# Optimization experiments

Measured on AMD Instinct MI355X. Metric: run time of the kernel, lower is better.

The kernel has to match this reference:

```python
import jax, jax.numpy as jnp
import numpy as np

T = 4096      # tokens (flattened batch*seq)
DIN = 2048    # input hidden dim
DQ = 2048     # q output dim
DKV = 2048    # per-head-group kv output dim (== DQ here, MHA)
NA = 4        # number of adapters (LoRA/delta models)
R = 16        # lora rank per q/k/v


def setup_inputs() -> dict:
    key = jax.random.key(0)
    ks = jax.random.split(key, 8)
    def rn(k, shape, scale):
        return jax.random.normal(k, shape, dtype=jnp.float32) * scale
    return {
        "x": rn(ks[0], (T, DIN), 1.0),
        "W_base": rn(ks[1], (DQ + 2 * DKV, DIN), DIN ** -0.5),
        "A_buffer_qkv": rn(ks[2], (NA, DIN, 3 * R), DIN ** -0.5),
        "B_buffer_q": rn(ks[3], (NA, R, DQ), R ** -0.5),
        "B_buffer_kv": rn(ks[4], (NA, R, 2 * DKV), R ** -0.5),
        "DeltaW_q": rn(ks[5], (NA, DIN, DQ), DIN ** -0.5),
        "DeltaW_kv": rn(ks[6], (NA, DIN, 2 * DKV), DIN ** -0.5),
        "weight_indices": jax.random.randint(ks[7], (T,), 0, NA, dtype=jnp.int32),
    }


def _ldmm(indices, x, A, B, D):
    """Per-token adapter-indexed (LoRA + dense delta) matmul.
    indices: [T] int, x: [T, din], A: [na, din, r], B: [na, r, dout], D: [na, din, dout].
    out[t] = (x[t] @ A[a]) @ B[a] + x[t] @ D[a]  with a = indices[t].
    Implemented as masked GEMMs over the small fixed adapter set.
    """
    na = A.shape[0]
    out = jnp.zeros((x.shape[0], B.shape[2]), dtype=x.dtype)
    for a in range(na):  # small fixed loop over adapters
        xa = jnp.where((indices == a)[:, None], x, jnp.zeros((), x.dtype))
        out = out + (xa @ A[a]) @ B[a] + xa @ D[a]
    return out


def reference(x, W_base, A_buffer_qkv, B_buffer_q, B_buffer_kv,
              DeltaW_q, DeltaW_kv, weight_indices):
    # base QKV projection (ColumnParallelLinear, no bias): [T, dq + 2*dkv]
    base = x @ W_base.T
    rank = A_buffer_qkv.shape[2] // 3
    b_dim_q = B_buffer_q.shape[2]
    b_dim_kv = B_buffer_kv.shape[2] // 2
    d_dim_kv = DeltaW_kv.shape[2] // 2
    for i in range(3):  # q, k, v slices
        if i == 0:
            o = _ldmm(weight_indices, x,
                      A_buffer_qkv[:, :, :rank], B_buffer_q, DeltaW_q)
            base = base.at[:, :b_dim_q].add(o)
        else:
            o = _ldmm(weight_indices, x,
                      A_buffer_qkv[:, :, i * rank:(i + 1) * rank],
                      B_buffer_kv[:, :, (i - 1) * b_dim_kv:i * b_dim_kv],
                      DeltaW_kv[:, :, (i - 1) * d_dim_kv:i * d_dim_kv])
            base = base.at[:, i * b_dim_kv:(i + 1) * b_dim_kv].add(o)
    return base
```

## Files before the change

kernel.cpp:

```cpp
#include <hip/hip_runtime.h>
#include <stdint.h>

#define T_TOK 4096
#define DIN   2048
#define DQ    2048
#define DKV   2048
#define NOUT  (DQ + 2*DKV)
#define NA    4
#define RLORA 16
#define BM    256
#define BN    256
#define MPAD  (T_TOK + NA*BM)
#define MTILES (MPAD/BM)
#define KX    (DIN + 64)
#define NKT64 (KX/64)
#define KSPLIT 16
#define NTBLK (NOUT/BN)
#define NWG   (MTILES*NTBLK)

typedef unsigned short u16;
typedef __attribute__((ext_vector_type(8))) short short8;
typedef __attribute__((ext_vector_type(8))) u16 u16x8;
typedef __attribute__((ext_vector_type(4))) float f32x4;

__device__ __forceinline__ u16 f2bf(float f) {
  uint32_t u = __float_as_uint(f);
  u = (u + 0x7FFFu + ((u >> 16) & 1u)) >> 16;
  return (u16)u;
}
__device__ __forceinline__ float bf2f(u16 u) {
  return __uint_as_float(((uint32_t)u) << 16);
}

typedef __attribute__((address_space(3))) void lds_void;
typedef __attribute__((address_space(1))) void glb_void;

__device__ __forceinline__ void gl_lds16(const void* g, void* l) {
  __builtin_amdgcn_global_load_lds((const glb_void*)(uintptr_t)g,
                                   (lds_void*)(uint32_t)(uintptr_t)l, 16, 0, 0);
}

__global__ void prep_kernel(const int* __restrict__ widx,
                            int* __restrict__ tok,
                            int* __restrict__ tileAdapter) {
  __shared__ int cnt[256][NA];
  __shared__ int total[NA];
  __shared__ int pad_off[NA];
  const int tid = threadIdx.x;
  const int CH = T_TOK / 256;
  const int base = tid * CH;
  int c[NA] = {0, 0, 0, 0};
  for (int i = 0; i < CH; i++) c[widx[base + i]]++;
  for (int a = 0; a < NA; a++) cnt[tid][a] = c[a];
  __syncthreads();
  if (tid < NA) {
    int s = 0;
    for (int i = 0; i < 256; i++) { int v = cnt[i][tid]; cnt[i][tid] = s; s += v; }
    total[tid] = s;
  }
  __syncthreads();
  if (tid == 0) {
    int off = 0;
    for (int a = 0; a < NA; a++) {
      pad_off[a] = off;
      int ntile = (total[a] + BM - 1) / BM;
      for (int tl = 0; tl < ntile; tl++) tileAdapter[off / BM + tl] = a;
      off += ntile * BM;
    }
    for (int tl = off / BM; tl < MTILES; tl++) tileAdapter[tl] = -1;
  }
  __syncthreads();
  for (int i = tid; i < MPAD; i += 256) tok[i] = -1;
  __syncthreads();
  int myoff[NA];
  for (int a = 0; a < NA; a++) myoff[a] = pad_off[a] + cnt[tid][a];
  for (int i = 0; i < CH; i++) {
    int a = widx[base + i];
    tok[myoff[a]++] = base + i;
  }
}

__global__ void gather_kernel(const float* __restrict__ x,
                              const int* __restrict__ tok,
                              u16* __restrict__ Xg) {
  const int row = blockIdx.x;
  const int t = tok[row];
  const int tid = threadIdx.x;
  u16x8* dst = (u16x8*)(Xg + (size_t)row * KX);
  if (t < 0) {
    u16x8 z = {0, 0, 0, 0, 0, 0, 0, 0};
    dst[tid] = z;
    return;
  }
  const f32x4* src = (const f32x4*)(x + (size_t)t * DIN);
  f32x4 v0 = src[tid * 2];
  f32x4 v1 = src[tid * 2 + 1];
  u16x8 o;
  o[0] = f2bf(v0[0]); o[1] = f2bf(v0[1]); o[2] = f2bf(v0[2]); o[3] = f2bf(v0[3]);
  o[4] = f2bf(v1[0]); o[5] = f2bf(v1[1]); o[6] = f2bf(v1[2]); o[7] = f2bf(v1[3]);
  dst[tid] = o;
}

__global__ __launch_bounds__(256) void xa_partial_kernel(
    const u16* __restrict__ Xg, const float* __restrict__ A_qkv,
    const int* __restrict__ tileAdapter, float* __restrict__ Ppart) {
  const int ks = blockIdx.y;
  const int ad = tileAdapter[blockIdx.x >> 1];
  const int a = ad < 0 ? 0 : ad;
  const int kb = ks * (DIN / KSPLIT);
  const int tid = threadIdx.x;
  const int rg = tid >> 2;
  const int jg = tid & 3;
  const int r0 = blockIdx.x * 128 + rg * 2;
  const int j0 = jg * 12;
  __shared__ float ldsA[64][56];
  float acc[2][12];
  #pragma unroll
  for (int r = 0; r < 2; r++)
    #pragma unroll
    for (int j = 0; j < 12; j++) acc[r][j] = 0.f;

  for (int kc = 0; kc < 2; kc++) {
    const int kbase = kb + kc * 64;
    for (int i = tid; i < 64 * 48; i += 256) {
      int kk = i / 48, j = i - kk * 48;
      ldsA[kk][j] = A_qkv[((size_t)a * DIN + kbase + kk) * (3 * RLORA) + j];
    }
    __syncthreads();
    u16x8 xr[2][8];
    #pragma unroll
    for (int r = 0; r < 2; r++)
      #pragma unroll
      for (int q = 0; q < 8; q++)
        xr[r][q] = *(const u16x8*)(Xg + (size_t)(r0 + r) * KX + kbase + q * 8);
    #pragma unroll
    for (int q = 0; q < 8; q++) {
      #pragma unroll
      for (int e = 0; e < 8; e++) {
        const int kk = q * 8 + e;
        f32x4 a0 = *(const f32x4*)&ldsA[kk][j0];
        f32x4 a1 = *(const f32x4*)&ldsA[kk][j0 + 4];
        f32x4 a2 = *(const f32x4*)&ldsA[kk][j0 + 8];
        float x0 = bf2f(xr[0][q][e]);
        float x1 = bf2f(xr[1][q][e]);
        #pragma unroll
        for (int c = 0; c < 4; c++) {
          acc[0][c]     += x0 * a0[c];  acc[1][c]     += x1 * a0[c];
          acc[0][4 + c] += x0 * a1[c];  acc[1][4 + c] += x1 * a1[c];
          acc[0][8 + c] += x0 * a2[c];  acc[1][8 + c] += x1 * a2[c];
        }
      }
    }
    __syncthreads();
  }
  #pragma unroll
  for (int r = 0; r < 2; r++)
    #pragma unroll
    for (int j = 0; j < 12; j++)
      Ppart[((size_t)ks * MPAD + r0 + r) * 48 + j0 + j] = acc[r][j];
}

__global__ void xa_reduce_kernel(const float* __restrict__ Ppart,
                                 u16* __restrict__ Xg) {
  const int gid = blockIdx.x * 256 + threadIdx.x;
  const int row = gid >> 6, j = gid & 63;
  float s = 0.f;
  if (j < 48) {
    #pragma unroll
    for (int sp = 0; sp < KSPLIT; sp++)
      s += Ppart[((size_t)sp * MPAD + row) * 48 + j];
  }
  Xg[(size_t)row * KX + DIN + j] = f2bf(s);
}

__global__ __launch_bounds__(256) void weff2_kernel(
    const float* __restrict__ W_base,
    const float* __restrict__ DW_q, const float* __restrict__ DW_kv,
    u16* __restrict__ Weff) {
  const int k0 = blockIdx.x * 64;
  const int n0 = blockIdx.y * 64;
  const int tid = threadIdx.x;
  const int k8 = (tid & 7) * 8;
  __shared__ float ldsD[64][65];

  f32x4 wb[2][2];
  #pragma unroll
  for (int h = 0; h < 2; h++) {
    const int nn = h * 32 + (tid >> 3);
    const float* p = W_base + (size_t)(n0 + nn) * DIN + k0 + k8;
    wb[h][0] = *(const f32x4*)p;
    wb[h][1] = *(const f32x4*)(p + 4);
  }

  const int ldD  = (n0 < DQ) ? DQ : 2 * DKV;
  const int ncol = (n0 < DQ) ? n0 : n0 - DQ;

  for (int a = 0; a < NA; a++) {
    const float* Dp = (n0 < DQ)
        ? DW_q  + (size_t)a * DIN * DQ + ncol
        : DW_kv + (size_t)a * DIN * (2 * DKV) + ncol;
    for (int i = tid; i < 64 * 64; i += 256) {
      int kk = i >> 6, nn2 = i & 63;
      ldsD[kk][nn2] = Dp[(size_t)(k0 + kk) * ldD + nn2];
    }
    __syncthreads();
    #pragma unroll
    for (int h = 0; h < 2; h++) {
      const int nn = h * 32 + (tid >> 3);
      u16x8 o;
      #pragma unroll
      for (int j = 0; j < 8; j++)
        o[j] = f2bf(wb[h][j >> 2][j & 3] + ldsD[k8 + j][nn]);
      *(u16x8*)(Weff + ((size_t)a * NOUT + n0 + nn) * KX + k0 + k8) = o;
    }
    __syncthreads();
  }
}

__global__ void wslots_kernel(const float* __restrict__ B_q,
                              const float* __restrict__ B_kv,
                              u16* __restrict__ Weff) {
  const int a = blockIdx.y;
  const int n = blockIdx.x * 256 + threadIdx.x;
  const int seg = n >> 11;
  u16 vals[64];
  #pragma unroll
  for (int j = 0; j < 64; j++) vals[j] = 0;
  if (seg == 0) {
    const float* Bp = B_q + ((size_t)a * RLORA) * DQ + n;
    #pragma unroll
    for (int r = 0; r < RLORA; r++) vals[r] = f2bf(Bp[(size_t)r * DQ]);
  } else if (seg == 1) {
    const float* Bp = B_kv + ((size_t)a * RLORA) * (2 * DKV) + (n - DQ);
    #pragma unroll
    for (int r = 0; r < RLORA; r++) vals[RLORA + r] = f2bf(Bp[(size_t)r * (2 * DKV)]);
  } else {
    const float* Bp = B_kv + ((size_t)a * RLORA) * (2 * DKV) + (n - DQ);
    #pragma unroll
    for (int r = 0; r < RLORA; r++) vals[2 * RLORA + r] = f2bf(Bp[(size_t)r * (2 * DKV)]);
  }
  u16* dst = Weff + ((size_t)a * NOUT + n) * KX + DIN;
  #pragma unroll
  for (int v = 0; v < 8; v++) *(u16x8*)(dst + v * 8) = *(u16x8*)(vals + v * 8);
}

#define BAR      asm volatile("s_barrier" ::: "memory")
#define WAITV(n) asm volatile("s_waitcnt vmcnt(" #n ")" ::: "memory")

#define RD_A(db, mh) { \
  _Pragma("unroll") for (int q = 0; q < 4; ++q) { \
    const char* rp = ldsc + (db)*32768 + (wm*128 + (mh)*64 + q*16 + fr)*128; \
    af[q][0] = *(const short8*)(rp + ck0); \
    af[q][1] = *(const short8*)(rp + ck1); } }

#define RD_B(db, nh, bfv) { \
  _Pragma("unroll") for (int q = 0; q < 2; ++q) { \
    const char* rp = ldsc + 65536 + (db)*32768 + ((nh)*128 + wn*32 + q*16 + fr)*128; \
    bfv[q][0] = *(const short8*)(rp + ck0); \
    bfv[q][1] = *(const short8*)(rp + ck1); } }

#define ST_A(db, mh, t) { \
  gl_lds16(gAsrc + (size_t)((mh)*64)*KX + (size_t)(t)*64, \
           ldsu + (db)*16384 + ((mh)*64*64) + stid); \
  gl_lds16(gAsrc + (size_t)(128 + (mh)*64)*KX + (size_t)(t)*64, \
           ldsu + (db)*16384 + ((128 + (mh)*64)*64) + stid); }

#define ST_B(db, nh, t) { \
  gl_lds16(gBsrc + (size_t)((nh)*32)*KX + (size_t)(t)*64, \
           ldsu + 32768 + (db)*16384 + ((nh)*128*64) + stid); \
  gl_lds16(gBsrc + (size_t)(128 + (nh)*32)*KX + (size_t)(t)*64, \
           ldsu + 32768 + (db)*16384 + (((nh)*128 + 64)*64) + stid); }

#define MM(mh, nh, bfv) { \
  __builtin_amdgcn_s_setprio(1); \
  _Pragma("unroll") for (int q = 0; q < 4; ++q) \
  _Pragma("unroll") for (int r = 0; r < 2; ++r) { \
    acc[(mh)*4+q][(nh)*2+r] = __builtin_amdgcn_mfma_f32_16x16x32_bf16( \
        af[q][0], bfv[r][0], acc[(mh)*4+q][(nh)*2+r], 0, 0, 0); \
    acc[(mh)*4+q][(nh)*2+r] = __builtin_amdgcn_mfma_f32_16x16x32_bf16( \
        af[q][1], bfv[r][1], acc[(mh)*4+q][(nh)*2+r], 0, 0, 0); } \
  __builtin_amdgcn_s_setprio(0); }

#define KT_STD(db, t) { \
  RD_A(db, 0); RD_B(db, 0, bf0); ST_A(1-(db), 1, (t)+1); BAR; MM(0, 0, bf0); BAR; \
  RD_B(db, 1, bf1);              ST_B(1-(db), 0, (t)+1); BAR; MM(0, 1, bf1); BAR; \
  RD_A(db, 1);                   ST_A(db, 0, (t)+2);     BAR; MM(1, 1, bf1); BAR; \
  ST_B(db, 1, (t)+2); WAITV(4);                          BAR; MM(1, 0, bf0); BAR; }

#define KT_T31(db, t) { \
  RD_A(db, 0); RD_B(db, 0, bf0); ST_A(1-(db), 1, (t)+1); BAR; MM(0, 0, bf0); BAR; \
  RD_B(db, 1, bf1);              ST_B(1-(db), 0, (t)+1); BAR; MM(0, 1, bf1); BAR; \
  RD_A(db, 1);                                           BAR; MM(1, 1, bf1); BAR; \
  WAITV(0);                                              BAR; MM(1, 0, bf0); BAR; }

#define KT_LAST(db) { \
  RD_A(db, 0); RD_B(db, 0, bf0); BAR; MM(0, 0, bf0); BAR; \
  RD_B(db, 1, bf1);              BAR; MM(0, 1, bf1); BAR; \
  RD_A(db, 1);                   BAR; MM(1, 1, bf1); BAR; \
                                 BAR; MM(1, 0, bf0); BAR; }

__global__ __launch_bounds__(512, 2) void gemm256_kernel(
    const u16* __restrict__ Xg, const u16* __restrict__ Weff,
    const int* __restrict__ tok, const int* __restrict__ tileAdapter,
    float* __restrict__ out) {
  __shared__ __align__(16) u16 Lds[65536];

  const int bid = blockIdx.x;
  const int wg = (bid & 7) * (NWG / 8) + (bid >> 3);
  const int mt = wg % MTILES, nt = wg / MTILES;
  const int a = tileAdapter[mt];
  if (a < 0) return;
  const int m0 = mt * BM, n0 = nt * BN;

  const int tid = threadIdx.x;
  const int l = tid & 63, w = tid >> 6;
  const int wm = w >> 2, wn = w & 3;
  const int fr = l & 15;
  const int kq = l >> 4;
  const int s7 = l & 7;
  const int ck0 = ((kq ^ s7) << 4);
  const int ck1 = (((4 + kq) ^ s7) << 4);

  const int l64 = tid >> 3;
  const int swc = (tid & 7) ^ (l64 & 7);
  const int stid = tid * 8;
  const u16* gAsrc = Xg + (size_t)(m0 + l64) * KX + swc * 8;
  const int nB = ((l64 >> 5) * 64) + (l64 & 31);
  const u16* gBsrc = Weff + ((size_t)a * NOUT + n0 + nB) * KX + swc * 8;

  u16* ldsu = &Lds[0];
  const char* ldsc = (const char*)ldsu;

  f32x4 acc[8][4];
  #pragma unroll
  for (int i = 0; i < 8; i++)
    #pragma unroll
    for (int j = 0; j < 4; j++) acc[i][j] = (f32x4){0.f, 0.f, 0.f, 0.f};

  short8 af[4][2], bf0[2][2], bf1[2][2];

  ST_A(0, 0, 0); ST_B(0, 0, 0); ST_A(0, 1, 0); ST_B(0, 1, 0);
  ST_A(1, 0, 1); ST_B(1, 1, 1);
  WAITV(4);
  BAR;

  for (int p = 0; p < 15; ++p) {
    const int t0 = 2 * p;
    KT_STD(0, t0);
    KT_STD(1, t0 + 1);
  }
  KT_STD(0, 30);
  KT_T31(1, 31);
  KT_LAST(0);

  #pragma unroll
  for (int mi = 0; mi < 8; ++mi) {
    const int rb = m0 + wm * 128 + mi * 16 + ((l >> 4) << 2);
    int tt[4];
    #pragma unroll
    for (int reg = 0; reg < 4; ++reg) tt[reg] = tok[rb + reg];
    #pragma unroll
    for (int ni = 0; ni < 4; ++ni) {
      const int col = n0 + wn * 64 + ni * 16 + fr;
      #pragma unroll
      for (int reg = 0; reg < 4; ++reg)
        if (tt[reg] >= 0) out[(size_t)tt[reg] * NOUT + col] = acc[mi][ni][reg];
    }
  }
}

__global__ void fallback_kernel(const float* __restrict__ x,
                                const float* __restrict__ W_base,
                                const float* __restrict__ A_qkv,
                                const float* __restrict__ B_q,
                                const float* __restrict__ B_kv,
                                const float* __restrict__ DW_q,
                                const float* __restrict__ DW_kv,
                                const int* __restrict__ widx,
                                float* __restrict__ out) {
  const int t = blockIdx.x;
  const int n = blockIdx.y * 256 + threadIdx.x;
  const int a = widx[t];
  __shared__ float xs[DIN];
  __shared__ float ys[3 * RLORA];
  for (int k = threadIdx.x; k < DIN; k += 256) xs[k] = x[(size_t)t * DIN + k];
  __syncthreads();
  if (threadIdx.x < 3 * RLORA) {
    float s = 0.f;
    const float* Ap = A_qkv + (size_t)a * DIN * (3 * RLORA) + threadIdx.x;
    for (int k = 0; k < DIN; k++) s += xs[k] * Ap[(size_t)k * (3 * RLORA)];
    ys[threadIdx.x] = s;
  }
  __syncthreads();
  const float* dcol; int ldD, roff; const float* bcol; int ldB;
  if (n < DQ) {
    dcol = DW_q + (size_t)a * DIN * DQ + n; ldD = DQ; roff = 0;
    bcol = B_q + (size_t)a * RLORA * DQ + n; ldB = DQ;
  } else {
    dcol = DW_kv + (size_t)a * DIN * (2 * DKV) + (n - DQ); ldD = 2 * DKV;
    roff = (n < 2 * DQ) ? RLORA : 2 * RLORA;
    bcol = B_kv + (size_t)a * RLORA * (2 * DKV) + (n - DQ); ldB = 2 * DKV;
  }
  const float* wrow = W_base + (size_t)n * DIN;
  float acc = 0.f;
  for (int k = 0; k < DIN; k++) acc += xs[k] * (wrow[k] + dcol[(size_t)k * ldD]);
  for (int r = 0; r < RLORA; r++) acc += ys[roff + r] * bcol[(size_t)r * ldB];
  out[(size_t)t * NOUT + n] = acc;
}

extern "C" void kernel_launch(void* const* d_in, const int* in_sizes, int n_in,
                              void* d_out, int out_size, void* d_ws, size_t ws_size,
                              hipStream_t stream) {
  const float* x      = (const float*)d_in[0];
  const float* W_base = (const float*)d_in[1];
  const float* A_qkv  = (const float*)d_in[2];
  const float* B_q    = (const float*)d_in[3];
  const float* B_kv   = (const float*)d_in[4];
  const float* DW_q   = (const float*)d_in[5];
  const float* DW_kv  = (const float*)d_in[6];
  const int*   widx   = (const int*)d_in[7];
  float* out = (float*)d_out;

  const size_t WEFF_BYTES = (size_t)NA * NOUT * KX * sizeof(u16);
  const size_t XG_BYTES   = (size_t)MPAD * KX * sizeof(u16);
  const size_t TOK_BYTES  = (size_t)MPAD * sizeof(int);
  const size_t TILE_BYTES = (size_t)MTILES * sizeof(int);
  const size_t need = WEFF_BYTES + XG_BYTES + TOK_BYTES + TILE_BYTES;

  if (ws_size < need) {
    fallback_kernel<<<dim3(T_TOK, NOUT / 256), 256, 0, stream>>>(
        x, W_base, A_qkv, B_q, B_kv, DW_q, DW_kv, widx, out);
    return;
  }

  char* ws = (char*)d_ws;
  u16* Weff = (u16*)ws;
  u16* Xg   = (u16*)(ws + WEFF_BYTES);
  int* tok  = (int*)(ws + WEFF_BYTES + XG_BYTES);
  int* tileAdapter = tok + MPAD;
  float* Ppart = (float*)ws;

  prep_kernel<<<1, 256, 0, stream>>>(widx, tok, tileAdapter);
  gather_kernel<<<MPAD, 256, 0, stream>>>(x, tok, Xg);
  xa_partial_kernel<<<dim3(MPAD / 128, KSPLIT), 256, 0, stream>>>(
      Xg, A_qkv, tileAdapter, Ppart);
  xa_reduce_kernel<<<MPAD * 64 / 256, 256, 0, stream>>>(Ppart, Xg);
  weff2_kernel<<<dim3(DIN / 64, NOUT / 64), 256, 0, stream>>>(
      W_base, DW_q, DW_kv, Weff);
  wslots_kernel<<<dim3(NOUT / 256, NA), 256, 0, stream>>>(B_q, B_kv, Weff);
  gemm256_kernel<<<dim3(NWG), 512, 0, stream>>>(
      Xg, Weff, tok, tileAdapter, out);
}
```

Baseline: 248.5 us.

## Prefetch next adapter delta tile in registers and regroup GEMM tile order

The weight-merge kernel now loads the next adapter's DeltaW tile into registers while the current tile is stored to LDS and converted. This overlaps global loads with the bf16 conversion and writes instead of running load, sync and compute in strict sequence. The GEMM kernel also remaps block IDs so each group walks pairs of M tiles across all N tiles, which is meant to improve L2 reuse of the X and weight tiles. Keeping 16 extra floats live per thread raises register pressure in the merge kernel.

```diff
diff --git a/kernel.cpp b/kernel.cpp
--- a/kernel.cpp
+++ b/kernel.cpp
@@ -194,14 +194,28 @@
 
   const int ldD  = (n0 < DQ) ? DQ : 2 * DKV;
   const int ncol = (n0 < DQ) ? n0 : n0 - DQ;
+  const float* Dbase = (n0 < DQ) ? (DW_q + ncol) : (DW_kv + ncol);
+  const size_t Dstride = (n0 < DQ) ? (size_t)DIN * DQ : (size_t)DIN * (2 * DKV);
+
+  const int lkk = tid >> 6;
+  const int lnn = tid & 63;
+
+  float v[16];
+  {
+    const float* Dp = Dbase;
+    #pragma unroll
+    for (int j = 0; j < 16; j++)
+      v[j] = Dp[(size_t)(k0 + lkk + 4 * j) * ldD + lnn];
+  }
 
   for (int a = 0; a < NA; a++) {
-    const float* Dp = (n0 < DQ)
-        ? DW_q  + (size_t)a * DIN * DQ + ncol
-        : DW_kv + (size_t)a * DIN * (2 * DKV) + ncol;
-    for (int i = tid; i < 64 * 64; i += 256) {
-      int kk = i >> 6, nn2 = i & 63;
-      ldsD[kk][nn2] = Dp[(size_t)(k0 + kk) * ldD + nn2];
+    #pragma unroll
+    for (int j = 0; j < 16; j++) ldsD[lkk + 4 * j][lnn] = v[j];
+    if (a < NA - 1) {
+      const float* Dp = Dbase + (size_t)(a + 1) * Dstride;
+      #pragma unroll
+      for (int j = 0; j < 16; j++)
+        v[j] = Dp[(size_t)(k0 + lkk + 4 * j) * ldD + lnn];
     }
     __syncthreads();
     #pragma unroll
@@ -306,8 +320,11 @@
   __shared__ __align__(16) u16 Lds[65536];
 
   const int bid = blockIdx.x;
-  const int wg = (bid & 7) * (NWG / 8) + (bid >> 3);
-  const int mt = wg % MTILES, nt = wg / MTILES;
+  const int lw = (bid & 7) * (NWG / 8) + (bid >> 3);
+  const int pg  = lw / (2 * NTBLK);
+  const int rem = lw % (2 * NTBLK);
+  const int nt  = rem >> 1;
+  const int mt  = pg * 2 + (rem & 1);
   const int a = tileAdapter[mt];
   if (a < 0) return;
   const int m0 = mt * BM, n0 = nt * BN;
```

Result: no change. 249.1 us (+0.2%).
